# Kernel optimization log

Measured on AMD Instinct MI355X. Metric: run time of the kernel, lower is better.

## Reference

```python
import jax, jax.numpy as jnp
import numpy as np

N, D, H = 1024, 256, 512


def _linear_init(key, fan_in, fan_out):
    kw, kb = jax.random.split(key)
    bound = 1.0 / np.sqrt(fan_in)
    w = jax.random.uniform(kw, (fan_in, fan_out), jnp.float32, -bound, bound)
    b = jax.random.uniform(kb, (fan_out,), jnp.float32, -bound, bound)
    return w, b


def setup_inputs() -> dict:
    key = jax.random.key(0)
    ks = jax.random.split(key, 8)
    domain_a = jax.random.normal(ks[0], (N, D), jnp.float32)
    domain_b = jax.random.normal(ks[1], (N, D), jnp.float32)
    mu_w0, mu_b0 = _linear_init(ks[2], D, H)
    mu_w1, mu_b1 = _linear_init(ks[3], H, H)
    mu_w2, mu_b2 = _linear_init(ks[4], H, D)
    lv_w0, lv_b0 = _linear_init(ks[5], D, H)
    lv_w1, lv_b1 = _linear_init(ks[6], H, H)
    lv_w2, lv_b2 = _linear_init(ks[7], H, D)
    return dict(domain_a=domain_a, domain_b=domain_b,
                mu_w0=mu_w0, mu_b0=mu_b0, mu_w1=mu_w1, mu_b1=mu_b1, mu_w2=mu_w2, mu_b2=mu_b2,
                lv_w0=lv_w0, lv_b0=lv_b0, lv_w1=lv_w1, lv_b1=lv_b1, lv_w2=lv_w2, lv_b2=lv_b2)


def _net(x, ws, bs, final_act):
    h = x
    for i in range(len(ws)):
        h = h @ ws[i] + bs[i]
        if i < len(ws) - 1:
            h = jax.nn.relu(h)
    return final_act(h)


def _l2norm(h):
    # L2NormEncoder == F.normalize(dim=-1), eps clamp like torch
    n = jnp.maximum(jnp.linalg.norm(h, axis=-1, keepdims=True), 1e-12)
    return h / n


def reference(domain_a, domain_b, mu_w0, mu_b0, mu_w1, mu_b1, mu_w2, mu_b2,
              lv_w0, lv_b0, lv_w1, lv_b1, lv_w2, lv_b2):
    mu_ws, mu_bs = [mu_w0, mu_w1, mu_w2], [mu_b0, mu_b1, mu_b2]
    lv_ws, lv_bs = [lv_w0, lv_w1, lv_w2], [lv_b0, lv_b1, lv_b2]

    # ---- embedding-model loss: prob-model params frozen (requires_grad=False) ----
    sg = jax.lax.stop_gradient
    mu = _net(domain_a, [sg(w) for w in mu_ws], [sg(b) for b in mu_bs], _l2norm)
    log_var = _net(domain_a, [sg(w) for w in lv_ws], [sg(b) for b in lv_bs], jnp.tanh)
    inv_var = jnp.exp(-log_var)                                  # [N, D]
    pos_probs = jnp.sum(-(domain_b - mu) ** 2 * inv_var - log_var, axis=-1)  # [N]
    # pairwise: [i, j, d] = b[j, d] - mu[i, d]; mean over j
    diff2_mean = jnp.mean((domain_b[None, :, :] - mu[:, None, :]) ** 2, axis=1)  # [N, D]
    neg_probs = jnp.sum(-diff2_mean * inv_var - log_var, axis=-1)  # [N]
    embed_model_loss = jnp.mean(pos_probs - neg_probs)

    # ---- prob-model loss: embeddings detached, params trainable ----
    a_d, b_d = sg(domain_a), sg(domain_b)
    mu2 = _net(a_d, mu_ws, mu_bs, _l2norm)
    lv2 = _net(a_d, lv_ws, lv_bs, jnp.tanh)
    prob_model_loss = jnp.mean(jnp.sum((b_d - mu2) ** 2 * jnp.exp(-lv2) + lv2, axis=-1))

    emb_coef, prob_coef = 1.0, 1.0
    loss = emb_coef * embed_model_loss + prob_coef * prob_model_loss
    return loss
```

## Files before the change

### kernel.cpp

```cpp
#include <hip/hip_runtime.h>
#include <hip/hip_fp16.h>

#define N_ROWS 1024
#define DIM 256
#define HID 512
#define CTR 16

typedef _Float16 half_t;
typedef __attribute__((ext_vector_type(4))) _Float16 half4v;
typedef __attribute__((ext_vector_type(8))) _Float16 half8v;
typedef __attribute__((ext_vector_type(16))) float f32x16;

struct Params {
    const float* a;
    const float* b;
    const float* w[6];
    const float* bias[6];
    unsigned* c1;
    unsigned* c2;
    unsigned* c3;
    float* acc;
    unsigned* done;
    float* ebsum;
    float* eb2sum;
    unsigned short* g_mu;
    unsigned short* g_lv;
    half_t* g_h1[2];
    half_t* g_h2[2];
    half_t* wt[6];
    float* out;
};

__global__ __launch_bounds__(256) void prep_kernel(Params p) {
    const int y = blockIdx.y, bx = blockIdx.x, tid = threadIdx.x;

    if (y == 6) {
        if (bx >= 64) return;
        const int d = tid, r0 = bx * 16;
        float s = 0.f, s2 = 0.f;
        #pragma unroll
        for (int r = 0; r < 16; ++r) {
            float v = p.b[(r0 + r) * DIM + d];
            s += v; s2 = fmaf(v, v, s2);
        }
        atomicAdd(&p.ebsum[d], s);
        atomicAdd(&p.eb2sum[d], s2);
        return;
    }
    __shared__ float T[32][33];
    const float* src = p.w[y];
    half_t* dst = p.wt[y];
    const int K = (y < 2) ? DIM : HID;
    const int N = (y < 4) ? HID : DIM;
    const int C = K >> 5;
    const int tilesN = N >> 5;
    if (bx >= C * tilesN) return;
    const int tk = bx / tilesN, tn = bx % tilesN;

    {
        const int r = tid >> 3, c4 = (tid & 7) * 4;
        float4 v = *(const float4*)&src[(tk * 32 + r) * N + tn * 32 + c4];
        T[r][c4 + 0] = v.x; T[r][c4 + 1] = v.y; T[r][c4 + 2] = v.z; T[r][c4 + 3] = v.w;
    }
    __syncthreads();
    const int which = tid >> 7;
    const int lane64 = (tid >> 1) & 63;
    const int epart = tid & 1;
    const int hi = lane64 >> 5, lr = lane64 & 31;
    const int rbase = which * 16 + hi * 8 + epart * 4;
    half4v h;
    h[0] = (half_t)T[rbase + 0][lr];
    h[1] = (half_t)T[rbase + 1][lr];
    h[2] = (half_t)T[rbase + 2][lr];
    h[3] = (half_t)T[rbase + 3][lr];
    *(half4v*)&dst[((tn * C + tk) * 2 + which) * 512 + lane64 * 8 + epart * 4] = h;
}

__device__ __forceinline__ void flag_add(unsigned* c) {
    asm volatile("s_waitcnt vmcnt(0)" ::: "memory");
    __syncthreads();
    if (threadIdx.x == 0)
        __hip_atomic_fetch_add(c, 1u, __ATOMIC_RELAXED, __HIP_MEMORY_SCOPE_AGENT);
}
__device__ __forceinline__ void flag_wait(unsigned* c, unsigned tgt) {
    if (threadIdx.x == 0) {
        while (__hip_atomic_load(c, __ATOMIC_RELAXED, __HIP_MEMORY_SCOPE_AGENT) < tgt)
            __builtin_amdgcn_s_sleep(1);
    }
    __syncthreads();
    asm volatile("" ::: "memory");
}

template <int KC>
__device__ __forceinline__ f32x16 mma_tile(const half_t* __restrict__ XA,
                                           const half_t* __restrict__ Wfrag,
                                           const int NCtot, const int tile,
                                           const int k0, const int lane) {
    const int lr = lane & 31, hi = lane >> 5;
    const int sa = (lr >> 3) & 3;
    const int aoff0 = lr * 40 + ((hi ^ sa) * 8);
    const int aoff1 = lr * 40 + (((hi + 2) ^ sa) * 8);
    const half_t* Wp = Wfrag + (tile * NCtot + k0) * 1024 + lane * 8;
    const half_t* Ap = XA + k0 * 1280;
    f32x16 acc;
    #pragma unroll
    for (int i = 0; i < 16; ++i) acc[i] = 0.f;
    #pragma unroll
    for (int c = 0; c < KC; ++c) {
        half8v av0 = *(const half8v*)&Ap[c * 1280 + aoff0];
        half8v av1 = *(const half8v*)&Ap[c * 1280 + aoff1];
        half8v bv0 = *(const half8v*)(Wp + c * 1024);
        half8v bv1 = *(const half8v*)(Wp + c * 1024 + 512);
        acc = __builtin_amdgcn_mfma_f32_32x32x16_f16(av0, bv0, acc, 0, 0, 0);
        acc = __builtin_amdgcn_mfma_f32_32x32x16_f16(av1, bv1, acc, 0, 0, 0);
    }
    return acc;
}

__device__ __forceinline__ void stage_a(const float* __restrict__ a, half_t* XA,
                                        const int R0, const int tid) {
    const int r = tid >> 4, q = tid & 15;
    const float* src = &a[(R0 + r) * DIM + q * 16];
    float4 v0 = *(const float4*)(src);
    float4 v1 = *(const float4*)(src + 4);
    float4 v2 = *(const float4*)(src + 8);
    float4 v3 = *(const float4*)(src + 12);
    half8v h0, h1;
    h0[0] = (half_t)v0.x; h0[1] = (half_t)v0.y; h0[2] = (half_t)v0.z; h0[3] = (half_t)v0.w;
    h0[4] = (half_t)v1.x; h0[5] = (half_t)v1.y; h0[6] = (half_t)v1.z; h0[7] = (half_t)v1.w;
    h1[0] = (half_t)v2.x; h1[1] = (half_t)v2.y; h1[2] = (half_t)v2.z; h1[3] = (half_t)v2.w;
    h1[4] = (half_t)v3.x; h1[5] = (half_t)v3.y; h1[6] = (half_t)v3.z; h1[7] = (half_t)v3.w;
    const int c = q >> 1, kb0 = (q & 1) * 2, sr = (r >> 3) & 3;
    *(half8v*)&XA[c * 1280 + r * 40 + ((kb0 ^ sr) * 8)] = h0;
    *(half8v*)&XA[c * 1280 + r * 40 + (((kb0 + 1) ^ sr) * 8)] = h1;
}

__device__ __forceinline__ void stage_h(const half_t* __restrict__ src, half_t* XA,
                                        const int R0, const int tid) {
    const int r = tid >> 4, q = tid & 15;
    const half_t* sp = &src[(R0 + r) * HID + q * 32];
    half8v x0 = *(const half8v*)(sp);
    half8v x1 = *(const half8v*)(sp + 8);
    half8v x2 = *(const half8v*)(sp + 16);
    half8v x3 = *(const half8v*)(sp + 24);
    const int sr = (r >> 3) & 3;
    half_t* d = &XA[q * 1280 + r * 40];
    *(half8v*)&d[(0 ^ sr) * 8] = x0;
    *(half8v*)&d[(1 ^ sr) * 8] = x1;
    *(half8v*)&d[(2 ^ sr) * 8] = x2;
    *(half8v*)&d[(3 ^ sr) * 8] = x3;
}

__device__ __forceinline__ void reduce2_wide(f32x16 acc, char* smem, int tl, int kh,
                                             int lane, int tid,
                                             const float* __restrict__ bias, int colbase,
                                             unsigned short* __restrict__ dstG, int Nout,
                                             int R0, bool relu) {
    float* redf = (float*)smem;
    half_t* redh = (half_t*)(smem + 24576);
    __syncthreads();
    if (kh) {
        #pragma unroll
        for (int i = 0; i < 16; ++i) redf[tl * 1024 + i * 64 + lane] = acc[i];
    }
    __syncthreads();
    if (!kh) {
        const int lr = lane & 31, hi = lane >> 5;
        const int coll = tl * 32 + lr;
        const float bv = bias[colbase + coll];
        #pragma unroll
        for (int i = 0; i < 16; ++i) {
            float v = acc[i] + redf[tl * 1024 + i * 64 + lane] + bv;
            if (relu) v = fmaxf(v, 0.f);
            const int row = (i & 3) + 8 * (i >> 2) + 4 * hi;
            redh[row * 136 + coll] = (half_t)v;
        }
    }
    __syncthreads();
    {
        const int row = tid >> 4, c8 = (tid & 15) * 8;
        const unsigned long long* sp = (const unsigned long long*)&redh[row * 136 + c8];
        unsigned long long v0 = sp[0], v1 = sp[1];
        unsigned long long* dp = (unsigned long long*)&dstG[(R0 + row) * Nout + colbase + c8];
        __hip_atomic_store(dp, v0, __ATOMIC_RELAXED, __HIP_MEMORY_SCOPE_AGENT);
        __hip_atomic_store(dp + 1, v1, __ATOMIC_RELAXED, __HIP_MEMORY_SCOPE_AGENT);
    }
}

__device__ __forceinline__ void reduce4_wide(f32x16 acc, char* smem, int tl, int kq,
                                             int lane, int tid,
                                             const float* __restrict__ bias, int colbase,
                                             unsigned short* __restrict__ dstG, int Nout,
                                             int R0) {
    float* redf = (float*)smem;
    half_t* redh = (half_t*)(smem + 24576);
    __syncthreads();
    if (kq) {
        #pragma unroll
        for (int i = 0; i < 16; ++i)
            redf[(tl * 3 + kq - 1) * 1024 + i * 64 + lane] = acc[i];
    }
    __syncthreads();
    if (!kq) {
        const int lr = lane & 31, hi = lane >> 5;
        const int coll = tl * 32 + lr;
        const float bv = bias[colbase + coll];
        #pragma unroll
        for (int i = 0; i < 16; ++i) {
            float v = acc[i] + bv
                    + redf[(tl * 3 + 0) * 1024 + i * 64 + lane]
                    + redf[(tl * 3 + 1) * 1024 + i * 64 + lane]
                    + redf[(tl * 3 + 2) * 1024 + i * 64 + lane];
            const int row = (i & 3) + 8 * (i >> 2) + 4 * hi;
            redh[row * 72 + coll] = (half_t)v;
        }
    }
    __syncthreads();
    {
        const int row = tid >> 4, c4 = (tid & 15) * 4;
        unsigned long long v0 = *(const unsigned long long*)&redh[row * 72 + c4];
        unsigned long long* dp = (unsigned long long*)&dstG[(R0 + row) * Nout + colbase + c4];
        __hip_atomic_store(dp, v0, __ATOMIC_RELAXED, __HIP_MEMORY_SCOPE_AGENT);
    }
}

__global__ void __launch_bounds__(512, 2) main_kernel(Params p) {
    __shared__ alignas(16) char smem[41024];
    half_t* XA = (half_t*)smem;
    float* bsum = (float*)(smem + 40960);

    const int bid = blockIdx.x, tid = threadIdx.x;
    const int net = bid & 1, g = (bid >> 1) & 31, s = bid >> 6;
    const int R0 = g * 32;
    const int w = tid >> 6, lane = tid & 63;

    stage_a(p.a, XA, R0, tid);
    __syncthreads();
    {
        const int tl = w >> 1, kh = w & 1;
        const int tile = s * 4 + tl;
        f32x16 acc = mma_tile<4>(XA, p.wt[net], 8, tile, kh * 4, lane);
        reduce2_wide(acc, smem, tl, kh, lane, tid, p.bias[net], s * 128,
                     (unsigned short*)p.g_h1[net], HID, R0, true);
    }
    flag_add(p.c1 + (net * 32 + g) * CTR);

    flag_wait(p.c1 + (net * 32 + g) * CTR, 4);
    stage_h(p.g_h1[net], XA, R0, tid);
    __syncthreads();
    {
        const int tl = w >> 1, kh = w & 1;
        const int tile = s * 4 + tl;
        f32x16 acc = mma_tile<8>(XA, p.wt[2 + net], 16, tile, kh * 8, lane);
        reduce2_wide(acc, smem, tl, kh, lane, tid, p.bias[2 + net], s * 128,
                     (unsigned short*)p.g_h2[net], HID, R0, true);
    }
    flag_add(p.c2 + (net * 32 + g) * CTR);

    flag_wait(p.c2 + (net * 32 + g) * CTR, 4);
    stage_h(p.g_h2[net], XA, R0, tid);
    __syncthreads();
    {
        const int tl = w >> 2, kq = w & 3;
        const int tile = s * 2 + tl;
        f32x16 acc = mma_tile<4>(XA, p.wt[4 + net], 16, tile, kq * 4, lane);
        reduce4_wide(acc, smem, tl, kq, lane, tid, p.bias[4 + net], s * 64,
                     net ? p.g_lv : p.g_mu, DIM, R0);
    }
    flag_add(p.c3 + g * CTR);

    if (net == 0) return;

    if (tid == 0) *bsum = 0.f;
    const int d0 = lane * 4;
    float4 ebf = *(const float4*)&p.ebsum[d0];
    float4 eb2f = *(const float4*)&p.eb2sum[d0];
    flag_wait(p.c3 + g * CTR, 8);

    const int i = R0 + s * 8 + w;
    const half_t* muP = (const half_t*)p.g_mu;
    const half_t* lvP = (const half_t*)p.g_lv;
    half4v mh = *(const half4v*)&muP[i * DIM + d0];
    half4v lh = *(const half4v*)&lvP[i * DIM + d0];
    const float invN = 1.0f / (float)N_ROWS;
    float m4[4] = {(float)mh[0], (float)mh[1], (float)mh[2], (float)mh[3]};
    float l4[4] = {(float)lh[0], (float)lh[1], (float)lh[2], (float)lh[3]};
    float eb[4] = {ebf.x * invN, ebf.y * invN, ebf.z * invN, ebf.w * invN};
    float eb2[4] = {eb2f.x * invN, eb2f.y * invN, eb2f.z * invN, eb2f.w * invN};

    float ss = 0.f;
    #pragma unroll
    for (int t = 0; t < 4; ++t) ss = fmaf(m4[t], m4[t], ss);
    #pragma unroll
    for (int o = 32; o > 0; o >>= 1) ss += __shfl_xor(ss, o, 64);
    const float inv_norm = 1.f / fmaxf(sqrtf(ss), 1e-12f);

    float wacc = 0.f;
    #pragma unroll
    for (int t = 0; t < 4; ++t) {
        float mu = m4[t] * inv_norm;
        float lv = tanhf(l4[t]);
        float iv = expf(-lv);
        float diff2 = fmaf(mu, mu, fmaf(-2.f * mu, eb[t], eb2[t]));
        wacc += fmaf(diff2, iv, lv);
    }
    #pragma unroll
    for (int o = 32; o > 0; o >>= 1) wacc += __shfl_xor(wacc, o, 64);
    if (lane == 0) atomicAdd(bsum, wacc);
    __syncthreads();
    if (tid == 0) {
        atomicAdd(p.acc, *bsum);
        asm volatile("s_waitcnt vmcnt(0)" ::: "memory");
        unsigned prev = __hip_atomic_fetch_add(p.done, 1u, __ATOMIC_RELAXED,
                                               __HIP_MEMORY_SCOPE_AGENT);
        if (prev == 127u) {
            float v = __hip_atomic_load(p.acc, __ATOMIC_RELAXED, __HIP_MEMORY_SCOPE_AGENT);
            p.out[0] = v * (1.0f / (float)N_ROWS);
        }
    }
}

extern "C" void kernel_launch(void* const* d_in, const int* in_sizes, int n_in,
                              void* d_out, int out_size, void* d_ws, size_t ws_size,
                              hipStream_t stream) {
    Params p;
    p.a = (const float*)d_in[0];
    p.b = (const float*)d_in[1];
    p.w[0] = (const float*)d_in[2];  p.bias[0] = (const float*)d_in[3];
    p.w[2] = (const float*)d_in[4];  p.bias[2] = (const float*)d_in[5];
    p.w[4] = (const float*)d_in[6];  p.bias[4] = (const float*)d_in[7];
    p.w[1] = (const float*)d_in[8];  p.bias[1] = (const float*)d_in[9];
    p.w[3] = (const float*)d_in[10]; p.bias[3] = (const float*)d_in[11];
    p.w[5] = (const float*)d_in[12]; p.bias[5] = (const float*)d_in[13];

    float* f = (float*)d_ws;
    p.c1   = (unsigned*)f;
    p.c2   = (unsigned*)(f + 1024);
    p.c3   = (unsigned*)(f + 2048);
    p.acc  = f + 2560;
    p.done = (unsigned*)(f + 2576);
    p.ebsum  = f + 2816;
    p.eb2sum = f + 3072;
    p.g_mu = (unsigned short*)(f + 4096);
    p.g_lv = (unsigned short*)(f + 4096 + 65536 * 2);
    half_t* hb = (half_t*)(f + 4096 + 65536 * 4);
    p.g_h1[0] = hb;  hb += N_ROWS * HID;
    p.g_h1[1] = hb;  hb += N_ROWS * HID;
    p.g_h2[0] = hb;  hb += N_ROWS * HID;
    p.g_h2[1] = hb;  hb += N_ROWS * HID;
    p.wt[0] = hb;  hb += HID * DIM;
    p.wt[1] = hb;  hb += HID * DIM;
    p.wt[2] = hb;  hb += HID * HID;
    p.wt[3] = hb;  hb += HID * HID;
    p.wt[4] = hb;  hb += DIM * HID;
    p.wt[5] = hb;  hb += DIM * HID;
    p.out = (float*)d_out;

    hipMemsetAsync(d_ws, 0, 16384, stream);
    prep_kernel<<<dim3(256, 7), 256, 0, stream>>>(p);
    main_kernel<<<256, 512, 0, stream>>>(p);
}
```

Before: 31.68 us.

## Keep layer-2 output in LDS and split layer-3 K across blocks with partial sums

Layer-2 activations now stay in shared memory instead of going to global memory. That removes the c2 flag barrier and the h2 global round trip. Layer 3 now computes split-K partial outputs in fp32 per block slice, and the final stage sums them. The b-column sums switch from atomics to per-block partials, and the hipMemsetAsync is replaced by zeroing inside prep_kernel. This costs more LDS per block, which may reduce occupancy, and adds fp32 partial-sum global traffic.

After: 38.73 us. +22.3%, slower.

```diff
diff --git a/kernel.cpp b/kernel.cpp
--- a/kernel.cpp
+++ b/kernel.cpp
@@ -17,16 +17,14 @@
     const float* w[6];
     const float* bias[6];
     unsigned* c1;
-    unsigned* c2;
     unsigned* c3;
     float* acc;
     unsigned* done;
-    float* ebsum;
-    float* eb2sum;
-    unsigned short* g_mu;
-    unsigned short* g_lv;
+    float* zbase;
+    float* part_s;
+    float* part_s2;
+    float* g_part;
     half_t* g_h1[2];
-    half_t* g_h2[2];
     half_t* wt[6];
     float* out;
 };
@@ -35,16 +33,20 @@
     const int y = blockIdx.y, bx = blockIdx.x, tid = threadIdx.x;
 
     if (y == 6) {
-        if (bx >= 64) return;
-        const int d = tid, r0 = bx * 16;
-        float s = 0.f, s2 = 0.f;
-        #pragma unroll
-        for (int r = 0; r < 16; ++r) {
-            float v = p.b[(r0 + r) * DIM + d];
-            s += v; s2 = fmaf(v, v, s2);
+        if (bx < 16) {
+            const int d = tid, r0 = bx * 64;
+            float s = 0.f, s2 = 0.f;
+            #pragma unroll 8
+            for (int r = 0; r < 64; ++r) {
+                float v = p.b[(r0 + r) * DIM + d];
+                s += v; s2 = fmaf(v, v, s2);
+            }
+            p.part_s[bx * 256 + d] = s;
+            p.part_s2[bx * 256 + d] = s2;
+        } else if (bx == 16) {
+            #pragma unroll
+            for (int k = 0; k < 8; ++k) p.zbase[tid + k * 256] = 0.f;
         }
-        atomicAdd(&p.ebsum[d], s);
-        atomicAdd(&p.eb2sum[d], s2);
         return;
     }
     __shared__ float T[32][33];
@@ -92,23 +94,20 @@
 }
 
 template <int KC>
-__device__ __forceinline__ f32x16 mma_tile(const half_t* __restrict__ XA,
-                                           const half_t* __restrict__ Wfrag,
-                                           const int NCtot, const int tile,
-                                           const int k0, const int lane) {
+__device__ __forceinline__ f32x16 mma_ab(const half_t* __restrict__ Ap0,
+                                         const half_t* __restrict__ Wp,
+                                         const int lane) {
     const int lr = lane & 31, hi = lane >> 5;
     const int sa = (lr >> 3) & 3;
     const int aoff0 = lr * 40 + ((hi ^ sa) * 8);
     const int aoff1 = lr * 40 + (((hi + 2) ^ sa) * 8);
-    const half_t* Wp = Wfrag + (tile * NCtot + k0) * 1024 + lane * 8;
-    const half_t* Ap = XA + k0 * 1280;
     f32x16 acc;
     #pragma unroll
     for (int i = 0; i < 16; ++i) acc[i] = 0.f;
     #pragma unroll
     for (int c = 0; c < KC; ++c) {
-        half8v av0 = *(const half8v*)&Ap[c * 1280 + aoff0];
-        half8v av1 = *(const half8v*)&Ap[c * 1280 + aoff1];
+        half8v av0 = *(const half8v*)(Ap0 + c * 1280 + aoff0);
+        half8v av1 = *(const half8v*)(Ap0 + c * 1280 + aoff1);
         half8v bv0 = *(const half8v*)(Wp + c * 1024);
         half8v bv1 = *(const half8v*)(Wp + c * 1024 + 512);
         acc = __builtin_amdgcn_mfma_f32_32x32x16_f16(av0, bv0, acc, 0, 0, 0);
@@ -151,13 +150,18 @@
     *(half8v*)&d[(3 ^ sr) * 8] = x3;
 }
 
-__device__ __forceinline__ void reduce2_wide(f32x16 acc, char* smem, int tl, int kh,
-                                             int lane, int tid,
-                                             const float* __restrict__ bias, int colbase,
-                                             unsigned short* __restrict__ dstG, int Nout,
-                                             int R0, bool relu) {
+#define OFF_H2C   40960
+#define OFF_REDH  51200
+#define OFF_BSUM  59904
+
+template <int TO_LDS>
+__device__ __forceinline__ void reduce2x(f32x16 acc, char* smem, int tl, int kh,
+                                         int lane, int tid,
+                                         const float* __restrict__ bias, int colbase,
+                                         unsigned short* __restrict__ dstG,
+                                         int R0) {
     float* redf = (float*)smem;
-    half_t* redh = (half_t*)(smem + 24576);
+    half_t* redh = (half_t*)(smem + OFF_REDH);
     __syncthreads();
     if (kh) {
         #pragma unroll
@@ -171,63 +175,34 @@
         #pragma unroll
         for (int i = 0; i < 16; ++i) {
             float v = acc[i] + redf[tl * 1024 + i * 64 + lane] + bv;
-            if (relu) v = fmaxf(v, 0.f);
+            v = fmaxf(v, 0.f);
             const int row = (i & 3) + 8 * (i >> 2) + 4 * hi;
             redh[row * 136 + coll] = (half_t)v;
         }
     }
     __syncthreads();
-    {
+    if (TO_LDS) {
+        half_t* H2C = (half_t*)(smem + OFF_H2C);
+        const int row = tid >> 4, c8 = (tid & 15) * 8;
+        half8v v = *(const half8v*)&redh[row * 136 + c8];
+        const int ch = c8 >> 5, kb = (c8 & 31) >> 3, sr = (row >> 3) & 3;
+        *(half8v*)&H2C[ch * 1280 + row * 40 + ((kb ^ sr) * 8)] = v;
+        __syncthreads();
+    } else {
         const int row = tid >> 4, c8 = (tid & 15) * 8;
         const unsigned long long* sp = (const unsigned long long*)&redh[row * 136 + c8];
         unsigned long long v0 = sp[0], v1 = sp[1];
-        unsigned long long* dp = (unsigned long long*)&dstG[(R0 + row) * Nout + colbase + c8];
+        unsigned long long* dp = (unsigned long long*)&dstG[(R0 + row) * HID + colbase + c8];
         __hip_atomic_store(dp, v0, __ATOMIC_RELAXED, __HIP_MEMORY_SCOPE_AGENT);
         __hip_atomic_store(dp + 1, v1, __ATOMIC_RELAXED, __HIP_MEMORY_SCOPE_AGENT);
     }
 }
 
-__device__ __forceinline__ void reduce4_wide(f32x16 acc, char* smem, int tl, int kq,
-                                             int lane, int tid,
-                                             const float* __restrict__ bias, int colbase,
-                                             unsigned short* __restrict__ dstG, int Nout,
-                                             int R0) {
-    float* redf = (float*)smem;
-    half_t* redh = (half_t*)(smem + 24576);
-    __syncthreads();
-    if (kq) {
-        #pragma unroll
-        for (int i = 0; i < 16; ++i)
-            redf[(tl * 3 + kq - 1) * 1024 + i * 64 + lane] = acc[i];
-    }
-    __syncthreads();
-    if (!kq) {
-        const int lr = lane & 31, hi = lane >> 5;
-        const int coll = tl * 32 + lr;
-        const float bv = bias[colbase + coll];
-        #pragma unroll
-        for (int i = 0; i < 16; ++i) {
-            float v = acc[i] + bv
-                    + redf[(tl * 3 + 0) * 1024 + i * 64 + lane]
-                    + redf[(tl * 3 + 1) * 1024 + i * 64 + lane]
-                    + redf[(tl * 3 + 2) * 1024 + i * 64 + lane];
-            const int row = (i & 3) + 8 * (i >> 2) + 4 * hi;
-            redh[row * 72 + coll] = (half_t)v;
-        }
-    }
-    __syncthreads();
-    {
-        const int row = tid >> 4, c4 = (tid & 15) * 4;
-        unsigned long long v0 = *(const unsigned long long*)&redh[row * 72 + c4];
-        unsigned long long* dp = (unsigned long long*)&dstG[(R0 + row) * Nout + colbase + c4];
-        __hip_atomic_store(dp, v0, __ATOMIC_RELAXED, __HIP_MEMORY_SCOPE_AGENT);
-    }
-}
-
 __global__ void __launch_bounds__(512, 2) main_kernel(Params p) {
-    __shared__ alignas(16) char smem[41024];
+    __shared__ alignas(16) char smem[59968];
     half_t* XA = (half_t*)smem;
-    float* bsum = (float*)(smem + 40960);
+    half_t* H2C = (half_t*)(smem + OFF_H2C);
+    float* bsum = (float*)(smem + OFF_BSUM);
 
     const int bid = blockIdx.x, tid = threadIdx.x;
     const int net = bid & 1, g = (bid >> 1) & 31, s = bid >> 6;
@@ -238,10 +213,11 @@
     __syncthreads();
     {
         const int tl = w >> 1, kh = w & 1;
-        const int tile = s * 4 + tl;
-        f32x16 acc = mma_tile<4>(XA, p.wt[net], 8, tile, kh * 4, lane);
-        reduce2_wide(acc, smem, tl, kh, lane, tid, p.bias[net], s * 128,
-                     (unsigned short*)p.g_h1[net], HID, R0, true);
+        f32x16 acc = mma_ab<4>(XA + kh * 4 * 1280,
+                               p.wt[net] + ((s * 4 + tl) * 8 + kh * 4) * 1024 + lane * 8,
+                               lane);
+        reduce2x<0>(acc, smem, tl, kh, lane, tid, p.bias[net], s * 128,
+                    (unsigned short*)p.g_h1[net], R0);
     }
     flag_add(p.c1 + (net * 32 + g) * CTR);
 
@@ -250,22 +226,39 @@
     __syncthreads();
     {
         const int tl = w >> 1, kh = w & 1;
-        const int tile = s * 4 + tl;
-        f32x16 acc = mma_tile<8>(XA, p.wt[2 + net], 16, tile, kh * 8, lane);
-        reduce2_wide(acc, smem, tl, kh, lane, tid, p.bias[2 + net], s * 128,
-                     (unsigned short*)p.g_h2[net], HID, R0, true);
-    }
-    flag_add(p.c2 + (net * 32 + g) * CTR);
-
-    flag_wait(p.c2 + (net * 32 + g) * CTR, 4);
-    stage_h(p.g_h2[net], XA, R0, tid);
-    __syncthreads();
+        f32x16 acc = mma_ab<8>(XA + kh * 8 * 1280,
+                               p.wt[2 + net] + ((s * 4 + tl) * 16 + kh * 8) * 1024 + lane * 8,
+                               lane);
+        reduce2x<1>(acc, smem, tl, kh, lane, tid, p.bias[2 + net], s * 128,
+                    nullptr, R0);
+    }
+
     {
-        const int tl = w >> 2, kq = w & 3;
-        const int tile = s * 2 + tl;
-        f32x16 acc = mma_tile<4>(XA, p.wt[4 + net], 16, tile, kq * 4, lane);
-        reduce4_wide(acc, smem, tl, kq, lane, tid, p.bias[4 + net], s * 64,
-                     net ? p.g_lv : p.g_mu, DIM, R0);
+        f32x16 acc = mma_ab<4>(H2C,
+                               p.wt[4 + net] + (w * 16 + s * 4) * 1024 + lane * 8,
+                               lane);
+        float* redf = (float*)smem;
+        #pragma unroll
+        for (int i = 0; i < 16; ++i) redf[w * 1024 + i * 64 + lane] = acc[i];
+        __syncthreads();
+        const int row = tid >> 4, c16 = (tid & 15) * 16;
+        const int i0 = (row & 3) | ((row >> 3) << 2);
+        const int hi2 = (row >> 2) & 1;
+        float* dst = p.g_part + (((net * 4 + s) * 1024) + R0 + row) * 256 + c16;
+        #pragma unroll
+        for (int jj = 0; jj < 8; ++jj) {
+            const int col0 = c16 + jj * 2;
+            union { float f2[2]; unsigned long long u; } cv;
+            #pragma unroll
+            for (int e = 0; e < 2; ++e) {
+                const int col = col0 + e;
+                float v = redf[(col >> 5) * 1024 + i0 * 64 + (col & 31) + 32 * hi2];
+                if (s == 0) v += p.bias[4 + net][col];
+                cv.f2[e] = v;
+            }
+            __hip_atomic_store((unsigned long long*)dst + jj, cv.u,
+                               __ATOMIC_RELAXED, __HIP_MEMORY_SCOPE_AGENT);
+        }
     }
     flag_add(p.c3 + g * CTR);
 
@@ -273,20 +266,29 @@
 
     if (tid == 0) *bsum = 0.f;
     const int d0 = lane * 4;
-    float4 ebf = *(const float4*)&p.ebsum[d0];
-    float4 eb2f = *(const float4*)&p.eb2sum[d0];
+    float eb[4] = {0.f, 0.f, 0.f, 0.f}, eb2[4] = {0.f, 0.f, 0.f, 0.f};
+    #pragma unroll
+    for (int j = 0; j < 16; ++j) {
+        float4 a4 = *(const float4*)&p.part_s[j * 256 + d0];
+        float4 b4 = *(const float4*)&p.part_s2[j * 256 + d0];
+        eb[0] += a4.x; eb[1] += a4.y; eb[2] += a4.z; eb[3] += a4.w;
+        eb2[0] += b4.x; eb2[1] += b4.y; eb2[2] += b4.z; eb2[3] += b4.w;
+    }
+    const float invN = 1.0f / (float)N_ROWS;
+    #pragma unroll
+    for (int t = 0; t < 4; ++t) { eb[t] *= invN; eb2[t] *= invN; }
+
     flag_wait(p.c3 + g * CTR, 8);
 
-    const int i = R0 + s * 8 + w;
-    const half_t* muP = (const half_t*)p.g_mu;
-    const half_t* lvP = (const half_t*)p.g_lv;
-    half4v mh = *(const half4v*)&muP[i * DIM + d0];
-    half4v lh = *(const half4v*)&lvP[i * DIM + d0];
-    const float invN = 1.0f / (float)N_ROWS;
-    float m4[4] = {(float)mh[0], (float)mh[1], (float)mh[2], (float)mh[3]};
-    float l4[4] = {(float)lh[0], (float)lh[1], (float)lh[2], (float)lh[3]};
-    float eb[4] = {ebf.x * invN, ebf.y * invN, ebf.z * invN, ebf.w * invN};
-    float eb2[4] = {eb2f.x * invN, eb2f.y * invN, eb2f.z * invN, eb2f.w * invN};
+    const int row = R0 + s * 8 + w;
+    float m4[4] = {0.f, 0.f, 0.f, 0.f}, l4[4] = {0.f, 0.f, 0.f, 0.f};
+    #pragma unroll
+    for (int s4 = 0; s4 < 4; ++s4) {
+        float4 mp = *(const float4*)&p.g_part[((s4) * 1024 + row) * 256 + d0];
+        float4 lp = *(const float4*)&p.g_part[((4 + s4) * 1024 + row) * 256 + d0];
+        m4[0] += mp.x; m4[1] += mp.y; m4[2] += mp.z; m4[3] += mp.w;
+        l4[0] += lp.x; l4[1] += lp.y; l4[2] += lp.z; l4[3] += lp.w;
+    }
 
     float ss = 0.f;
     #pragma unroll
@@ -334,20 +336,17 @@
     p.w[5] = (const float*)d_in[12]; p.bias[5] = (const float*)d_in[13];
 
     float* f = (float*)d_ws;
-    p.c1   = (unsigned*)f;
-    p.c2   = (unsigned*)(f + 1024);
-    p.c3   = (unsigned*)(f + 2048);
-    p.acc  = f + 2560;
-    p.done = (unsigned*)(f + 2576);
-    p.ebsum  = f + 2816;
-    p.eb2sum = f + 3072;
-    p.g_mu = (unsigned short*)(f + 4096);
-    p.g_lv = (unsigned short*)(f + 4096 + 65536 * 2);
-    half_t* hb = (half_t*)(f + 4096 + 65536 * 4);
+    p.c1    = (unsigned*)f;
+    p.c3    = (unsigned*)(f + 1024);
+    p.acc   = f + 1536;
+    p.done  = (unsigned*)(f + 1552);
+    p.zbase = f;
+    p.part_s  = f + 4096;
+    p.part_s2 = f + 8192;
+    p.g_part  = f + 16384;
+    half_t* hb = (half_t*)(f + 16384 + 2 * 4 * 1024 * 256);
     p.g_h1[0] = hb;  hb += N_ROWS * HID;
     p.g_h1[1] = hb;  hb += N_ROWS * HID;
-    p.g_h2[0] = hb;  hb += N_ROWS * HID;
-    p.g_h2[1] = hb;  hb += N_ROWS * HID;
     p.wt[0] = hb;  hb += HID * DIM;
     p.wt[1] = hb;  hb += HID * DIM;
     p.wt[2] = hb;  hb += HID * HID;
@@ -356,7 +355,6 @@
     p.wt[5] = hb;  hb += DIM * HID;
     p.out = (float*)d_out;
 
-    hipMemsetAsync(d_ws, 0, 16384, stream);
     prep_kernel<<<dim3(256, 7), 256, 0, stream>>>(p);
     main_kernel<<<256, 512, 0, stream>>>(p);
 }
```

## Drop memset, use per-wave flags, prefetch next-layer weights, partial-sum column stats

Applied to the files above, without the earlier changes.

Removes the host memset by zeroing the counters inside prep_kernel, and replaces the atomicAdd column sums of b with per-block partials that the main kernel reduces into LDS. Flag signalling becomes per-wave (no block barrier before the atomic), and each block preloads the first weight fragments of the next layer into registers before waiting on the cross-block flag. The aim is fewer launches, less barrier and atomic overhead, and weight-load latency hidden behind the wait. In exchange there are more registers (launch bounds no longer request 2 blocks per CU) and a redundant partial-sum reduction in every net-1 block.

After: 30.08 us (median of 3 runs). 1.05x faster.

```diff
diff --git a/kernel.cpp b/kernel.cpp
--- a/kernel.cpp
+++ b/kernel.cpp
@@ -21,8 +21,9 @@
     unsigned* c3;
     float* acc;
     unsigned* done;
-    float* ebsum;
-    float* eb2sum;
+    float* zbase;
+    float* part_s;
+    float* part_s2;
     unsigned short* g_mu;
     unsigned short* g_lv;
     half_t* g_h1[2];
@@ -35,16 +36,20 @@
     const int y = blockIdx.y, bx = blockIdx.x, tid = threadIdx.x;
 
     if (y == 6) {
-        if (bx >= 64) return;
-        const int d = tid, r0 = bx * 16;
-        float s = 0.f, s2 = 0.f;
-        #pragma unroll
-        for (int r = 0; r < 16; ++r) {
-            float v = p.b[(r0 + r) * DIM + d];
-            s += v; s2 = fmaf(v, v, s2);
+        if (bx < 64) {
+            const int d = tid, r0 = bx * 16;
+            float s = 0.f, s2 = 0.f;
+            #pragma unroll
+            for (int r = 0; r < 16; ++r) {
+                float v = p.b[(r0 + r) * DIM + d];
+                s += v; s2 = fmaf(v, v, s2);
+            }
+            p.part_s[bx * 256 + d] = s;
+            p.part_s2[bx * 256 + d] = s2;
+        } else if (bx == 64) {
+            #pragma unroll
+            for (int k = 0; k < 12; ++k) p.zbase[tid + k * 256] = 0.f;
         }
-        atomicAdd(&p.ebsum[d], s);
-        atomicAdd(&p.eb2sum[d], s2);
         return;
     }
     __shared__ float T[32][33];
@@ -76,10 +81,9 @@
     *(half4v*)&dst[((tn * C + tk) * 2 + which) * 512 + lane64 * 8 + epart * 4] = h;
 }
 
-__device__ __forceinline__ void flag_add(unsigned* c) {
+__device__ __forceinline__ void flag_add_wave(unsigned* c) {
     asm volatile("s_waitcnt vmcnt(0)" ::: "memory");
-    __syncthreads();
-    if (threadIdx.x == 0)
+    if ((threadIdx.x & 63) == 0)
         __hip_atomic_fetch_add(c, 1u, __ATOMIC_RELAXED, __HIP_MEMORY_SCOPE_AGENT);
 }
 __device__ __forceinline__ void flag_wait(unsigned* c, unsigned tgt) {
@@ -91,26 +95,23 @@
     asm volatile("" ::: "memory");
 }
 
-template <int KC>
-__device__ __forceinline__ f32x16 mma_tile(const half_t* __restrict__ XA,
-                                           const half_t* __restrict__ Wfrag,
-                                           const int NCtot, const int tile,
-                                           const int k0, const int lane) {
+template <int KC, int PRE>
+__device__ __forceinline__ f32x16 mma_pre(const half_t* __restrict__ Ap0,
+                                          const half_t* __restrict__ Wp,
+                                          const half8v (*wpre)[2], const int lane) {
     const int lr = lane & 31, hi = lane >> 5;
     const int sa = (lr >> 3) & 3;
     const int aoff0 = lr * 40 + ((hi ^ sa) * 8);
     const int aoff1 = lr * 40 + (((hi + 2) ^ sa) * 8);
-    const half_t* Wp = Wfrag + (tile * NCtot + k0) * 1024 + lane * 8;
-    const half_t* Ap = XA + k0 * 1280;
     f32x16 acc;
     #pragma unroll
     for (int i = 0; i < 16; ++i) acc[i] = 0.f;
     #pragma unroll
     for (int c = 0; c < KC; ++c) {
-        half8v av0 = *(const half8v*)&Ap[c * 1280 + aoff0];
-        half8v av1 = *(const half8v*)&Ap[c * 1280 + aoff1];
-        half8v bv0 = *(const half8v*)(Wp + c * 1024);
-        half8v bv1 = *(const half8v*)(Wp + c * 1024 + 512);
+        half8v av0 = *(const half8v*)(Ap0 + c * 1280 + aoff0);
+        half8v av1 = *(const half8v*)(Ap0 + c * 1280 + aoff1);
+        half8v bv0 = (c < PRE) ? wpre[c][0] : *(const half8v*)(Wp + c * 1024);
+        half8v bv1 = (c < PRE) ? wpre[c][1] : *(const half8v*)(Wp + c * 1024 + 512);
         acc = __builtin_amdgcn_mfma_f32_32x32x16_f16(av0, bv0, acc, 0, 0, 0);
         acc = __builtin_amdgcn_mfma_f32_32x32x16_f16(av1, bv1, acc, 0, 0, 0);
     }
@@ -151,13 +152,17 @@
     *(half8v*)&d[(3 ^ sr) * 8] = x3;
 }
 
+#define OFF_REDH  24576
+#define OFF_EB    41024
+#define OFF_BSUM  43072
+
 __device__ __forceinline__ void reduce2_wide(f32x16 acc, char* smem, int tl, int kh,
                                              int lane, int tid,
                                              const float* __restrict__ bias, int colbase,
-                                             unsigned short* __restrict__ dstG, int Nout,
+                                             unsigned short* __restrict__ dstG,
                                              int R0, bool relu) {
     float* redf = (float*)smem;
-    half_t* redh = (half_t*)(smem + 24576);
+    half_t* redh = (half_t*)(smem + OFF_REDH);
     __syncthreads();
     if (kh) {
         #pragma unroll
@@ -181,7 +186,7 @@
         const int row = tid >> 4, c8 = (tid & 15) * 8;
         const unsigned long long* sp = (const unsigned long long*)&redh[row * 136 + c8];
         unsigned long long v0 = sp[0], v1 = sp[1];
-        unsigned long long* dp = (unsigned long long*)&dstG[(R0 + row) * Nout + colbase + c8];
+        unsigned long long* dp = (unsigned long long*)&dstG[(R0 + row) * HID + colbase + c8];
         __hip_atomic_store(dp, v0, __ATOMIC_RELAXED, __HIP_MEMORY_SCOPE_AGENT);
         __hip_atomic_store(dp + 1, v1, __ATOMIC_RELAXED, __HIP_MEMORY_SCOPE_AGENT);
     }
@@ -190,10 +195,10 @@
 __device__ __forceinline__ void reduce4_wide(f32x16 acc, char* smem, int tl, int kq,
                                              int lane, int tid,
                                              const float* __restrict__ bias, int colbase,
-                                             unsigned short* __restrict__ dstG, int Nout,
+                                             unsigned short* __restrict__ dstG,
                                              int R0) {
     float* redf = (float*)smem;
-    half_t* redh = (half_t*)(smem + 24576);
+    half_t* redh = (half_t*)(smem + OFF_REDH);
     __syncthreads();
     if (kq) {
         #pragma unroll
@@ -219,74 +224,95 @@
     {
         const int row = tid >> 4, c4 = (tid & 15) * 4;
         unsigned long long v0 = *(const unsigned long long*)&redh[row * 72 + c4];
-        unsigned long long* dp = (unsigned long long*)&dstG[(R0 + row) * Nout + colbase + c4];
+        unsigned long long* dp = (unsigned long long*)&dstG[(R0 + row) * DIM + colbase + c4];
         __hip_atomic_store(dp, v0, __ATOMIC_RELAXED, __HIP_MEMORY_SCOPE_AGENT);
     }
 }
 
-__global__ void __launch_bounds__(512, 2) main_kernel(Params p) {
-    __shared__ alignas(16) char smem[41024];
+__global__ void __launch_bounds__(512) main_kernel(Params p) {
+    __shared__ alignas(16) char smem[43136];
     half_t* XA = (half_t*)smem;
-    float* bsum = (float*)(smem + 40960);
+    float* ebL  = (float*)(smem + OFF_EB);
+    float* eb2L = ebL + 256;
+    float* bsum = (float*)(smem + OFF_BSUM);
 
     const int bid = blockIdx.x, tid = threadIdx.x;
     const int net = bid & 1, g = (bid >> 1) & 31, s = bid >> 6;
     const int R0 = g * 32;
     const int w = tid >> 6, lane = tid & 63;
 
+    half8v wpre[4][2];
+
     stage_a(p.a, XA, R0, tid);
     __syncthreads();
     {
         const int tl = w >> 1, kh = w & 1;
-        const int tile = s * 4 + tl;
-        f32x16 acc = mma_tile<4>(XA, p.wt[net], 8, tile, kh * 4, lane);
+        const half_t* Wp = p.wt[net] + ((s * 4 + tl) * 8 + kh * 4) * 1024 + lane * 8;
+        f32x16 acc = mma_pre<4, 0>(XA + kh * 4 * 1280, Wp, nullptr, lane);
         reduce2_wide(acc, smem, tl, kh, lane, tid, p.bias[net], s * 128,
-                     (unsigned short*)p.g_h1[net], HID, R0, true);
-    }
-    flag_add(p.c1 + (net * 32 + g) * CTR);
-
-    flag_wait(p.c1 + (net * 32 + g) * CTR, 4);
+                     (unsigned short*)p.g_h1[net], R0, true);
+    }
+    flag_add_wave(p.c1 + (net * 32 + g) * CTR);
+
+    const int tl2 = w >> 1, kh2 = w & 1;
+    const half_t* WpL1 = p.wt[2 + net] + ((s * 4 + tl2) * 16 + kh2 * 8) * 1024 + lane * 8;
+    #pragma unroll
+    for (int c = 0; c < 4; ++c) {
+        wpre[c][0] = *(const half8v*)(WpL1 + c * 1024);
+        wpre[c][1] = *(const half8v*)(WpL1 + c * 1024 + 512);
+    }
+    flag_wait(p.c1 + (net * 32 + g) * CTR, 32);
     stage_h(p.g_h1[net], XA, R0, tid);
     __syncthreads();
     {
-        const int tl = w >> 1, kh = w & 1;
-        const int tile = s * 4 + tl;
-        f32x16 acc = mma_tile<8>(XA, p.wt[2 + net], 16, tile, kh * 8, lane);
-        reduce2_wide(acc, smem, tl, kh, lane, tid, p.bias[2 + net], s * 128,
-                     (unsigned short*)p.g_h2[net], HID, R0, true);
-    }
-    flag_add(p.c2 + (net * 32 + g) * CTR);
-
-    flag_wait(p.c2 + (net * 32 + g) * CTR, 4);
+        f32x16 acc = mma_pre<8, 4>(XA + kh2 * 8 * 1280, WpL1, wpre, lane);
+        reduce2_wide(acc, smem, tl2, kh2, lane, tid, p.bias[2 + net], s * 128,
+                     (unsigned short*)p.g_h2[net], R0, true);
+    }
+    flag_add_wave(p.c2 + (net * 32 + g) * CTR);
+
+    const int tl3 = w >> 2, kq3 = w & 3;
+    const half_t* WpL2 = p.wt[4 + net] + ((s * 2 + tl3) * 16 + kq3 * 4) * 1024 + lane * 8;
+    #pragma unroll
+    for (int c = 0; c < 4; ++c) {
+        wpre[c][0] = *(const half8v*)(WpL2 + c * 1024);
+        wpre[c][1] = *(const half8v*)(WpL2 + c * 1024 + 512);
+    }
+    flag_wait(p.c2 + (net * 32 + g) * CTR, 32);
     stage_h(p.g_h2[net], XA, R0, tid);
     __syncthreads();
     {
-        const int tl = w >> 2, kq = w & 3;
-        const int tile = s * 2 + tl;
-        f32x16 acc = mma_tile<4>(XA, p.wt[4 + net], 16, tile, kq * 4, lane);
-        reduce4_wide(acc, smem, tl, kq, lane, tid, p.bias[4 + net], s * 64,
-                     net ? p.g_lv : p.g_mu, DIM, R0);
-    }
-    flag_add(p.c3 + g * CTR);
+        f32x16 acc = mma_pre<4, 4>(XA + kq3 * 4 * 1280, WpL2, wpre, lane);
+        reduce4_wide(acc, smem, tl3, kq3, lane, tid, p.bias[4 + net], s * 64,
+                     net ? p.g_lv : p.g_mu, R0);
+    }
+    flag_add_wave(p.c3 + g * CTR);
 
     if (net == 0) return;
 
     if (tid == 0) *bsum = 0.f;
+    {
+        const int which = tid >> 8, d = tid & 255;
+        const float* P = which ? p.part_s2 : p.part_s;
+        float ssum = 0.f;
+        #pragma unroll 8
+        for (int j = 0; j < 64; ++j) ssum += P[j * 256 + d];
+        (which ? eb2L : ebL)[d] = ssum * (1.0f / (float)N_ROWS);
+    }
+    flag_wait(p.c3 + g * CTR, 64);
+
+    const int i = R0 + s * 8 + w;
     const int d0 = lane * 4;
-    float4 ebf = *(const float4*)&p.ebsum[d0];
-    float4 eb2f = *(const float4*)&p.eb2sum[d0];
-    flag_wait(p.c3 + g * CTR, 8);
-
-    const int i = R0 + s * 8 + w;
     const half_t* muP = (const half_t*)p.g_mu;
     const half_t* lvP = (const half_t*)p.g_lv;
     half4v mh = *(const half4v*)&muP[i * DIM + d0];
     half4v lh = *(const half4v*)&lvP[i * DIM + d0];
-    const float invN = 1.0f / (float)N_ROWS;
+    float4 ebf = *(const float4*)&ebL[d0];
+    float4 eb2f = *(const float4*)&eb2L[d0];
     float m4[4] = {(float)mh[0], (float)mh[1], (float)mh[2], (float)mh[3]};
     float l4[4] = {(float)lh[0], (float)lh[1], (float)lh[2], (float)lh[3]};
-    float eb[4] = {ebf.x * invN, ebf.y * invN, ebf.z * invN, ebf.w * invN};
-    float eb2[4] = {eb2f.x * invN, eb2f.y * invN, eb2f.z * invN, eb2f.w * invN};
+    float eb[4] = {ebf.x, ebf.y, ebf.z, ebf.w};
+    float eb2[4] = {eb2f.x, eb2f.y, eb2f.z, eb2f.w};
 
     float ss = 0.f;
     #pragma unroll
@@ -334,16 +360,17 @@
     p.w[5] = (const float*)d_in[12]; p.bias[5] = (const float*)d_in[13];
 
     float* f = (float*)d_ws;
-    p.c1   = (unsigned*)f;
-    p.c2   = (unsigned*)(f + 1024);
-    p.c3   = (unsigned*)(f + 2048);
-    p.acc  = f + 2560;
-    p.done = (unsigned*)(f + 2576);
-    p.ebsum  = f + 2816;
-    p.eb2sum = f + 3072;
-    p.g_mu = (unsigned short*)(f + 4096);
-    p.g_lv = (unsigned short*)(f + 4096 + 65536 * 2);
-    half_t* hb = (half_t*)(f + 4096 + 65536 * 4);
+    p.c1    = (unsigned*)f;
+    p.c2    = (unsigned*)(f + 1024);
+    p.c3    = (unsigned*)(f + 2048);
+    p.acc   = f + 2560;
+    p.done  = (unsigned*)(f + 2576);
+    p.zbase = f;
+    p.part_s  = f + 4096;
+    p.part_s2 = f + 20480;
+    p.g_mu = (unsigned short*)(f + 36864);
+    p.g_lv = p.g_mu + N_ROWS * DIM;
+    half_t* hb = (half_t*)(p.g_lv + N_ROWS * DIM);
     p.g_h1[0] = hb;  hb += N_ROWS * HID;
     p.g_h1[1] = hb;  hb += N_ROWS * HID;
     p.g_h2[0] = hb;  hb += N_ROWS * HID;
@@ -356,7 +383,6 @@
     p.wt[5] = hb;  hb += DIM * HID;
     p.out = (float*)d_out;
 
-    hipMemsetAsync(d_ws, 0, 16384, stream);
     prep_kernel<<<dim3(256, 7), 256, 0, stream>>>(p);
     main_kernel<<<256, 512, 0, stream>>>(p);
 }
```
